# Performance work log

Hardware: AMD Instinct MI355X
Metric: run time of the kernel (lower is better)

The kernel has to match this reference:

```python
import jax, jax.numpy as jnp
import numpy as np

N = 8192
N_DIM = 7
N_WIDTH = 64


def setup_inputs() -> dict:
    key = jax.random.key(0)
    ks = jax.random.split(key, 12)
    scale = 0.05
    u = lambda k, shape: scale * (2.0 * jax.random.uniform(k, shape) - 1.0)
    # Linear params stored as (in, out) so forward uses x @ W + b (same math as torch Linear).
    lin = lambda k, fan_in, fan_out: (
        jax.random.uniform(jax.random.fold_in(k, 0), (fan_in, fan_out),
                           minval=-1.0, maxval=1.0) / np.sqrt(fan_in),
        jax.random.uniform(jax.random.fold_in(k, 1), (fan_out,),
                           minval=-1.0, maxval=1.0) / np.sqrt(fan_in),
    )
    W1, b1 = lin(ks[1], N_DIM, N_WIDTH)
    W2, b2 = lin(ks[2], N_WIDTH, N_WIDTH)
    Wl, bl = lin(ks[3], N_WIDTH, 1)
    return {
        "x": jax.random.normal(ks[0], (N, N_DIM), dtype=jnp.float32),
        "alpha": jax.random.uniform(ks[4], (1,)),          # Edges.alpha = 1 * rand(1)
        "W1": W1, "b1": b1, "wt1": u(ks[5], (N_WIDTH, N_WIDTH)), "bs1": u(ks[6], (1,)),
        "W2": W2, "b2": b2, "wt2": u(ks[7], (N_WIDTH, N_WIDTH)), "bs2": u(ks[8], (1,)),
        "Wl": Wl, "bl": bl,
    }


def _edges(x, alpha):
    eta, phi = x[:, 1], x[:, 2]
    deta = eta[:, None] - eta[None, :]                      # (n, n)
    dphi = jnp.abs(phi[:, None] - phi[None, :])
    dphi = jnp.where(dphi > jnp.pi, 2.0 * jnp.pi - dphi, dphi)
    dRdR = deta * deta + dphi * dphi
    A = jnp.exp(-alpha[0] * dRdR)
    return jax.nn.softmax(A, axis=1) + jnp.eye(x.shape[0], dtype=x.dtype)


def _gcn_layer(X, A, W, b, wt, bs):
    X = jax.nn.relu(X @ W + b)                              # embed + relu
    X = (A @ X) @ wt + bs[0]                                # aggregate + mix + scalar bias
    return jax.nn.relu(X)


def reference(x, alpha, W1, b1, wt1, bs1, W2, b2, wt2, bs2, Wl, bl):
    A = _edges(x, alpha)
    V = jax.nn.relu(_gcn_layer(x, A, W1, b1, wt1, bs1))
    V = jax.nn.relu(_gcn_layer(V, A, W2, b2, wt2, bs2))
    s = V.sum(axis=0)                                       # (n_width,)
    return jax.nn.sigmoid(s @ Wl + bl)                      # (1,)
```

## Files before the change

kernel.cpp:

```cpp
#include <hip/hip_runtime.h>
#include <math.h>

#define NN 8192
#define L2E 1.44269504088896340736f
#define TWO_PI 6.28318530717958647693f

typedef _Float16 h8 __attribute__((ext_vector_type(8)));
typedef _Float16 h4 __attribute__((ext_vector_type(4)));
typedef float f32x4 __attribute__((ext_vector_type(4)));
typedef float f32x2 __attribute__((ext_vector_type(2)));
#define MFMA16(A, B, C) __builtin_amdgcn_mfma_f32_16x16x32_f16(A, B, C, 0, 0, 0)

union V8 { float4 v[2]; float f[8]; };

__global__ __launch_bounds__(256) void prep_kernel(
    const float* __restrict__ x, const float* __restrict__ alpha,
    const float* __restrict__ W1, const float* __restrict__ b1,
    float* __restrict__ eta_s, float* __restrict__ phi_s,
    float* __restrict__ H1, _Float16* __restrict__ HT1,
    float* __restrict__ svec)
{
  __shared__ float sW[448];
  __shared__ float sb[64];
  __shared__ float T[32][68];
  const int t = threadIdx.x;
  if (blockIdx.x == 0 && t < 64) svec[t] = 0.f;
  for (int k = t; k < 448; k += 256) sW[k] = W1[k];
  if (t < 64) sb[t] = b1[t];
  const float s = sqrtf(alpha[0] * L2E);
  const int i0 = blockIdx.x * 32;
  const int r = t >> 3, q = t & 7;
  const int i = i0 + r;
  float xv[7];
#pragma unroll
  for (int k = 0; k < 7; k++) xv[k] = x[i * 7 + k];
  if (q == 0) { eta_s[i] = xv[1] * s; phi_s[i] = xv[2] * s; }
  __syncthreads();
#pragma unroll
  for (int c = 0; c < 8; c++) {
    const int n = q * 8 + c;
    float hv = sb[n];
#pragma unroll
    for (int k = 0; k < 7; k++) hv = fmaf(xv[k], sW[k * 64 + n], hv);
    T[r][n] = fmaxf(hv, 0.f);
  }
  __syncthreads();
  for (int e = t; e < 512; e += 256)
    *(f32x4*)(H1 + (size_t)i0 * 64 + (e << 2)) =
        *(const f32x4*)&T[e >> 4][(e << 2) & 63];
  const int n = t >> 2, sg = (t & 3) * 8;
  h8 v;
#pragma unroll
  for (int ss = 0; ss < 8; ss++) v[ss] = (_Float16)T[sg + ss][n];
  *(h8*)(HT1 + (size_t)n * NN + i0 + sg) = v;
}

template <bool NEED_L>
__global__ __launch_bounds__(256, 4) void attn_pass(
    const float* __restrict__ eta_s, const float* __restrict__ phi_s,
    const _Float16* __restrict__ HT, const float* __restrict__ alpha,
    float* __restrict__ Ypart, float* __restrict__ lpart)
{
  __shared__ __align__(16) float smem[2 * 32 * 66];
  const int tid = threadIdx.x;
  const int w = tid >> 6, lane = tid & 63, m = lane & 15, g = lane >> 4;
  const int tile = blockIdx.x >> 2, part = blockIdx.x & 3;
  const int i0 = tile << 5;
  const int jbase = part << 11;
  const float Cs = TWO_PI * sqrtf(alpha[0] * L2E);
  const float et0 = eta_s[i0 + m],      ph0 = phi_s[i0 + m];
  const float et1 = eta_s[i0 + 16 + m], ph1 = phi_s[i0 + 16 + m];

  const int joff = jbase + (w << 5) + (g << 3);
  const _Float16* hb0 = HT + (size_t)m * NN + joff;
  const _Float16* hb1 = hb0 + (size_t)16 * NN;
  const _Float16* hb2 = hb0 + (size_t)32 * NN;
  const _Float16* hb3 = hb0 + (size_t)48 * NN;
  const float* ep = eta_s + joff;
  const float* pp = phi_s + joff;

  f32x4 a00 = {0,0,0,0}, a01 = {0,0,0,0}, a02 = {0,0,0,0}, a03 = {0,0,0,0};
  f32x4 a10 = {0,0,0,0}, a11 = {0,0,0,0}, a12 = {0,0,0,0}, a13 = {0,0,0,0};
  f32x4 l0a = {0,0,0,0}, l1a = {0,0,0,0};
  const h8 onesv = {(_Float16)1.f, (_Float16)1.f, (_Float16)1.f, (_Float16)1.f,
                    (_Float16)1.f, (_Float16)1.f, (_Float16)1.f, (_Float16)1.f};

  union AF { h8 v; decltype(__builtin_amdgcn_cvt_pkrtz(0.f, 0.f)) p[4]; };

#pragma unroll
  for (int s = 0; s < 16; ++s) {
    const h8 b0 = *(const h8*)(hb0 + s * 128);
    const h8 b1 = *(const h8*)(hb1 + s * 128);
    const h8 b2 = *(const h8*)(hb2 + s * 128);
    const h8 b3 = *(const h8*)(hb3 + s * 128);
    V8 E, P;
    E.v[0] = *(const float4*)(ep + s * 128);
    E.v[1] = *(const float4*)(ep + s * 128 + 4);
    P.v[0] = *(const float4*)(pp + s * 128);
    P.v[1] = *(const float4*)(pp + s * 128 + 4);

    AF af0, af1;
#pragma unroll
    for (int tt = 0; tt < 8; tt += 2) {
      const f32x2 pj = {P.f[tt], P.f[tt + 1]};
      const f32x2 ej = {E.f[tt], E.f[tt + 1]};
      const f32x2 dp0 = ph0 - pj, dp1 = ph1 - pj;
      const f32x2 ad0 = {fabsf(dp0.x), fabsf(dp0.y)};
      const f32x2 ad1 = {fabsf(dp1.x), fabsf(dp1.y)};
      const f32x2 cm0 = Cs - ad0, cm1 = Cs - ad1;
      const f32x2 wr0 = {fminf(ad0.x, cm0.x), fminf(ad0.y, cm0.y)};
      const f32x2 wr1 = {fminf(ad1.x, cm1.x), fminf(ad1.y, cm1.y)};
      const f32x2 de0 = et0 - ej, de1 = et1 - ej;
      const f32x2 r20 = de0 * de0 + wr0 * wr0;
      const f32x2 r21 = de1 * de1 + wr1 * wr1;
      const f32x2 ax0 = {__builtin_amdgcn_exp2f(-r20.x),
                         __builtin_amdgcn_exp2f(-r20.y)};
      const f32x2 ax1 = {__builtin_amdgcn_exp2f(-r21.x),
                         __builtin_amdgcn_exp2f(-r21.y)};
      const f32x2 ga0 = ax0 * L2E - L2E;
      const f32x2 ga1 = ax1 * L2E - L2E;
      af0.p[tt >> 1] = __builtin_amdgcn_cvt_pkrtz(
          __builtin_amdgcn_exp2f(ga0.x), __builtin_amdgcn_exp2f(ga0.y));
      af1.p[tt >> 1] = __builtin_amdgcn_cvt_pkrtz(
          __builtin_amdgcn_exp2f(ga1.x), __builtin_amdgcn_exp2f(ga1.y));
    }
    a00 = MFMA16(af0.v, b0, a00); a01 = MFMA16(af0.v, b1, a01);
    a02 = MFMA16(af0.v, b2, a02); a03 = MFMA16(af0.v, b3, a03);
    a10 = MFMA16(af1.v, b0, a10); a11 = MFMA16(af1.v, b1, a11);
    a12 = MFMA16(af1.v, b2, a12); a13 = MFMA16(af1.v, b3, a13);
    if constexpr (NEED_L) {
      l0a = MFMA16(af0.v, onesv, l0a);
      l1a = MFMA16(af1.v, onesv, l1a);
    }
  }

  typedef float Red2[32][66];
  Red2* red = (Red2*)smem;
  const int h = w >> 1;
  if ((w & 1) == 0) {
#pragma unroll
    for (int r = 0; r < 4; ++r) {
      red[h][g * 4 + r][m]      = a00[r]; red[h][g * 4 + r][16 + m] = a01[r];
      red[h][g * 4 + r][32 + m] = a02[r]; red[h][g * 4 + r][48 + m] = a03[r];
      red[h][16 + g * 4 + r][m]      = a10[r]; red[h][16 + g * 4 + r][16 + m] = a11[r];
      red[h][16 + g * 4 + r][32 + m] = a12[r]; red[h][16 + g * 4 + r][48 + m] = a13[r];
    }
    if constexpr (NEED_L) {
      if (m == 0) {
#pragma unroll
        for (int r = 0; r < 4; ++r) {
          red[h][g * 4 + r][64]      = l0a[r];
          red[h][16 + g * 4 + r][64] = l1a[r];
        }
      }
    }
  }
  __syncthreads();
  if (w & 1) {
#pragma unroll
    for (int r = 0; r < 4; ++r) {
      red[h][g * 4 + r][m]      += a00[r]; red[h][g * 4 + r][16 + m] += a01[r];
      red[h][g * 4 + r][32 + m] += a02[r]; red[h][g * 4 + r][48 + m] += a03[r];
      red[h][16 + g * 4 + r][m]      += a10[r]; red[h][16 + g * 4 + r][16 + m] += a11[r];
      red[h][16 + g * 4 + r][32 + m] += a12[r]; red[h][16 + g * 4 + r][48 + m] += a13[r];
    }
    if constexpr (NEED_L) {
      if (m == 0) {
#pragma unroll
        for (int r = 0; r < 4; ++r) {
          red[h][g * 4 + r][64]      += l0a[r];
          red[h][16 + g * 4 + r][64] += l1a[r];
        }
      }
    }
  }
  __syncthreads();
#pragma unroll
  for (int k = 0; k < 8; ++k) {
    const int e = tid + k * 256;
    Ypart[((size_t)part * NN + i0 + (e >> 6)) * 64 + (e & 63)] =
        red[0][e >> 6][e & 63] + red[1][e >> 6][e & 63];
  }
  if constexpr (NEED_L) {
    if (tid < 32)
      lpart[(size_t)part * NN + i0 + tid] = red[0][tid][64] + red[1][tid][64];
  }
}

__global__ __launch_bounds__(256) void mid_kernel(
    const float* __restrict__ Yp, const float* __restrict__ lp,
    const float* __restrict__ H1, const float* __restrict__ wt1,
    const float* __restrict__ bs1, const float* __restrict__ W2,
    const float* __restrict__ b2, float* __restrict__ H2,
    _Float16* __restrict__ HT2)
{
  __shared__ float sA[64][68];
  __shared__ float sB[64][68];
  __shared__ float U[16][68];
  __shared__ float sb2v[64];
  const int t = threadIdx.x;
  for (int e = t; e < 1024; e += 256) {
    const int rr = e >> 4, cc = (e << 2) & 63;
    *(f32x4*)&sA[rr][cc] = *(const f32x4*)(wt1 + (e << 2));
    *(f32x4*)&sB[rr][cc] = *(const f32x4*)(W2 + (e << 2));
  }
  if (t < 64) sb2v[t] = b2[t];
  const float bsv = bs1[0];
  const int i0 = blockIdx.x * 16;
  const int r = t >> 4, q = t & 15;
  const int i = i0 + r;
  float l = 0.f;
#pragma unroll
  for (int p = 0; p < 4; ++p) l += lp[(size_t)p * NN + i];
  const float rl = 1.0f / l;
  f32x4 ya = {0, 0, 0, 0};
#pragma unroll
  for (int p = 0; p < 4; ++p)
    ya += *(const f32x4*)(Yp + ((size_t)p * NN + i) * 64 + q * 4);
  const f32x4 h1 = *(const f32x4*)(H1 + (size_t)i * 64 + q * 4);
#pragma unroll
  for (int c = 0; c < 4; ++c) U[r][q * 4 + c] = fmaf(ya[c], rl, h1[c]);
  __syncthreads();
  float z[4];
#pragma unroll
  for (int c = 0; c < 4; ++c) z[c] = bsv;
#pragma unroll
  for (int k4 = 0; k4 < 64; k4 += 4) {
    const f32x4 u4 = *(const f32x4*)&U[r][k4];
#pragma unroll
    for (int kk = 0; kk < 4; ++kk) {
      const f32x4 sa = *(const f32x4*)&sA[k4 + kk][q * 4];
#pragma unroll
      for (int c = 0; c < 4; ++c) z[c] = fmaf(u4[kk], sa[c], z[c]);
    }
  }
  __syncthreads();
#pragma unroll
  for (int c = 0; c < 4; ++c) U[r][q * 4 + c] = fmaxf(z[c], 0.f);
  __syncthreads();
  float hv[4];
#pragma unroll
  for (int c = 0; c < 4; ++c) hv[c] = sb2v[q * 4 + c];
#pragma unroll
  for (int k4 = 0; k4 < 64; k4 += 4) {
    const f32x4 u4 = *(const f32x4*)&U[r][k4];
#pragma unroll
    for (int kk = 0; kk < 4; ++kk) {
      const f32x4 sb4 = *(const f32x4*)&sB[k4 + kk][q * 4];
#pragma unroll
      for (int c = 0; c < 4; ++c) hv[c] = fmaf(u4[kk], sb4[c], hv[c]);
    }
  }
  __syncthreads();
#pragma unroll
  for (int c = 0; c < 4; ++c) U[r][q * 4 + c] = fmaxf(hv[c], 0.f);
  __syncthreads();
  *(f32x4*)(H2 + (size_t)i0 * 64 + (t << 2)) =
      *(const f32x4*)&U[t >> 4][(t << 2) & 63];
  const int n = t >> 2, sg = (t & 3) * 4;
  h4 v;
#pragma unroll
  for (int ss = 0; ss < 4; ss++) v[ss] = (_Float16)U[sg + ss][n];
  *(h4*)(HT2 + (size_t)n * NN + i0 + sg) = v;
}

__global__ __launch_bounds__(256) void final_kernel(
    const float* __restrict__ Yp, const float* __restrict__ lp,
    const float* __restrict__ H2, const float* __restrict__ wt2,
    const float* __restrict__ bs2, float* __restrict__ svec)
{
  __shared__ float sA[64][68];
  __shared__ float U[16][68];
  __shared__ float cred[4][64];
  const int t = threadIdx.x;
  for (int e = t; e < 1024; e += 256) {
    const int rr = e >> 4, cc = (e << 2) & 63;
    *(f32x4*)&sA[rr][cc] = *(const f32x4*)(wt2 + (e << 2));
  }
  const float bsv = bs2[0];
  const int i0 = blockIdx.x * 16;
  const int r = t >> 4, q = t & 15;
  const int i = i0 + r;
  float l = 0.f;
#pragma unroll
  for (int p = 0; p < 4; ++p) l += lp[(size_t)p * NN + i];
  const float rl = 1.0f / l;
  f32x4 ya = {0, 0, 0, 0};
#pragma unroll
  for (int p = 0; p < 4; ++p)
    ya += *(const f32x4*)(Yp + ((size_t)p * NN + i) * 64 + q * 4);
  const f32x4 h2 = *(const f32x4*)(H2 + (size_t)i * 64 + q * 4);
#pragma unroll
  for (int c = 0; c < 4; ++c) U[r][q * 4 + c] = fmaf(ya[c], rl, h2[c]);
  __syncthreads();
  float z[4];
#pragma unroll
  for (int c = 0; c < 4; ++c) z[c] = bsv;
#pragma unroll
  for (int k4 = 0; k4 < 64; k4 += 4) {
    const f32x4 u4 = *(const f32x4*)&U[r][k4];
#pragma unroll
    for (int kk = 0; kk < 4; ++kk) {
      const f32x4 sa = *(const f32x4*)&sA[k4 + kk][q * 4];
#pragma unroll
      for (int c = 0; c < 4; ++c) z[c] = fmaf(u4[kk], sa[c], z[c]);
    }
  }
  __syncthreads();
#pragma unroll
  for (int c = 0; c < 4; ++c) U[r][q * 4 + c] = fmaxf(z[c], 0.f);
  __syncthreads();
  const int col = t & 63, rg = t >> 6;
  float ps = 0.f;
#pragma unroll
  for (int rr = 0; rr < 4; rr++) ps += U[rg * 4 + rr][col];
  cred[rg][col] = ps;
  __syncthreads();
  if (t < 64)
    atomicAdd(svec + t, cred[0][t] + cred[1][t] + cred[2][t] + cred[3][t]);
}

__global__ void out_kernel(const float* __restrict__ svec,
                           const float* __restrict__ Wl,
                           const float* __restrict__ bl,
                           float* __restrict__ out)
{
  const int t = threadIdx.x;
  float v = svec[t] * Wl[t];
#pragma unroll
  for (int off = 32; off > 0; off >>= 1) v += __shfl_down(v, off);
  if (t == 0) {
    const float logit = v + bl[0];
    out[0] = 1.0f / (1.0f + __builtin_amdgcn_exp2f(-logit * L2E));
  }
}

extern "C" void kernel_launch(void* const* d_in, const int* in_sizes, int n_in,
                              void* d_out, int out_size, void* d_ws,
                              size_t ws_size, hipStream_t stream)
{
  const float* x     = (const float*)d_in[0];
  const float* alpha = (const float*)d_in[1];
  const float* W1    = (const float*)d_in[2];
  const float* b1    = (const float*)d_in[3];
  const float* wt1   = (const float*)d_in[4];
  const float* bs1   = (const float*)d_in[5];
  const float* W2    = (const float*)d_in[6];
  const float* b2    = (const float*)d_in[7];
  const float* wt2   = (const float*)d_in[8];
  const float* bs2   = (const float*)d_in[9];
  const float* Wl    = (const float*)d_in[10];
  const float* bl    = (const float*)d_in[11];
  float* out = (float*)d_out;

  char* ws = (char*)d_ws;
  size_t off = 0;
  auto alloc = [&](size_t bytes) {
    void* p = ws + off;
    off = (off + bytes + 255) & ~(size_t)255;
    return p;
  };
  float* eta_s = (float*)alloc(NN * 4 + 256);
  float* phi_s = (float*)alloc(NN * 4 + 256);
  float* H1    = (float*)alloc((size_t)NN * 64 * 4);
  float* H2    = (float*)alloc((size_t)NN * 64 * 4);
  float* Ypart = (float*)alloc((size_t)4 * NN * 64 * 4);
  float* lpart = (float*)alloc((size_t)4 * NN * 4);
  _Float16* HT = (_Float16*)alloc((size_t)NN * 64 * 2 + 512);
  float* svec  = (float*)alloc(64 * 4);

  prep_kernel<<<256, 256, 0, stream>>>(x, alpha, W1, b1, eta_s, phi_s, H1, HT, svec);
  attn_pass<true><<<1024, 256, 0, stream>>>(eta_s, phi_s, HT, alpha, Ypart, lpart);
  mid_kernel<<<512, 256, 0, stream>>>(Ypart, lpart, H1, wt1, bs1, W2, b2, H2, HT);
  attn_pass<false><<<1024, 256, 0, stream>>>(eta_s, phi_s, HT, alpha, Ypart, nullptr);
  final_kernel<<<512, 256, 0, stream>>>(Ypart, lpart, H2, wt2, bs2, svec);
  out_kernel<<<1, 64, 0, stream>>>(svec, Wl, bl, out);
}
```

Before: 187.4 us.

## Double-buffer HT tiles via direct global-to-LDS loads in attention pass

The attention pass now streams the fp16 HT operand tiles into a per-wave double-buffered LDS slab with global_load_lds. The next step's eta/phi values are prefetched into registers while the current step computes, with explicit vmcnt waits and sched barriers controlling the overlap. The goal is to hide global load latency behind the exp/MFMA work. In exchange, the kernel uses 32 KB of shared memory per block, which may limit occupancy against the 4-blocks launch bound, and correctness depends on hand-tuned waitcnt values.

```diff
diff --git a/kernel.cpp b/kernel.cpp
--- a/kernel.cpp
+++ b/kernel.cpp
@@ -10,6 +10,11 @@
 typedef float f32x4 __attribute__((ext_vector_type(4)));
 typedef float f32x2 __attribute__((ext_vector_type(2)));
 #define MFMA16(A, B, C) __builtin_amdgcn_mfma_f32_16x16x32_f16(A, B, C, 0, 0, 0)
+
+#define GLD_LDS16(gsrc, ldst)                                          \
+  __builtin_amdgcn_global_load_lds(                                    \
+      (const __attribute__((address_space(1))) unsigned int*)(gsrc),   \
+      (__attribute__((address_space(3))) unsigned int*)(ldst), 16, 0, 0)
 
 union V8 { float4 v[2]; float f[8]; };
 
@@ -61,7 +66,7 @@
     const _Float16* __restrict__ HT, const float* __restrict__ alpha,
     float* __restrict__ Ypart, float* __restrict__ lpart)
 {
-  __shared__ __align__(16) float smem[2 * 32 * 66];
+  __shared__ __align__(16) char smem[32768];
   const int tid = threadIdx.x;
   const int w = tid >> 6, lane = tid & 63, m = lane & 15, g = lane >> 4;
   const int tile = blockIdx.x >> 2, part = blockIdx.x & 3;
@@ -72,12 +77,11 @@
   const float et1 = eta_s[i0 + 16 + m], ph1 = phi_s[i0 + 16 + m];
 
   const int joff = jbase + (w << 5) + (g << 3);
-  const _Float16* hb0 = HT + (size_t)m * NN + joff;
-  const _Float16* hb1 = hb0 + (size_t)16 * NN;
-  const _Float16* hb2 = hb0 + (size_t)32 * NN;
-  const _Float16* hb3 = hb0 + (size_t)48 * NN;
+  const _Float16* hb = HT + (size_t)m * NN + joff;
   const float* ep = eta_s + joff;
   const float* pp = phi_s + joff;
+
+  char* const slab = smem + (w << 13);
 
   f32x4 a00 = {0,0,0,0}, a01 = {0,0,0,0}, a02 = {0,0,0,0}, a03 = {0,0,0,0};
   f32x4 a10 = {0,0,0,0}, a11 = {0,0,0,0}, a12 = {0,0,0,0}, a13 = {0,0,0,0};
@@ -85,19 +89,42 @@
   const h8 onesv = {(_Float16)1.f, (_Float16)1.f, (_Float16)1.f, (_Float16)1.f,
                     (_Float16)1.f, (_Float16)1.f, (_Float16)1.f, (_Float16)1.f};
 
+  V8 Eb[2], Pb[2];
+
+#pragma unroll
+  for (int k = 0; k < 4; ++k)
+    GLD_LDS16(hb + (size_t)k * 16 * NN, slab + (k << 10));
+  Eb[0].v[0] = *(const float4*)(ep);     Eb[0].v[1] = *(const float4*)(ep + 4);
+  Pb[0].v[0] = *(const float4*)(pp);     Pb[0].v[1] = *(const float4*)(pp + 4);
+  __builtin_amdgcn_sched_barrier(0);
+
   union AF { h8 v; decltype(__builtin_amdgcn_cvt_pkrtz(0.f, 0.f)) p[4]; };
 
 #pragma unroll
   for (int s = 0; s < 16; ++s) {
-    const h8 b0 = *(const h8*)(hb0 + s * 128);
-    const h8 b1 = *(const h8*)(hb1 + s * 128);
-    const h8 b2 = *(const h8*)(hb2 + s * 128);
-    const h8 b3 = *(const h8*)(hb3 + s * 128);
-    V8 E, P;
-    E.v[0] = *(const float4*)(ep + s * 128);
-    E.v[1] = *(const float4*)(ep + s * 128 + 4);
-    P.v[0] = *(const float4*)(pp + s * 128);
-    P.v[1] = *(const float4*)(pp + s * 128 + 4);
+    if (s < 15) {
+      char* const nb = slab + (((s + 1) & 1) << 12);
+      const _Float16* src = hb + (s + 1) * 128;
+#pragma unroll
+      for (int k = 0; k < 4; ++k)
+        GLD_LDS16(src + (size_t)k * 16 * NN, nb + (k << 10));
+      Eb[(s + 1) & 1].v[0] = *(const float4*)(ep + (s + 1) * 128);
+      Eb[(s + 1) & 1].v[1] = *(const float4*)(ep + (s + 1) * 128 + 4);
+      Pb[(s + 1) & 1].v[0] = *(const float4*)(pp + (s + 1) * 128);
+      Pb[(s + 1) & 1].v[1] = *(const float4*)(pp + (s + 1) * 128 + 4);
+    }
+    __builtin_amdgcn_sched_barrier(0);
+    if (s < 15) asm volatile("s_waitcnt vmcnt(8)" ::: "memory");
+    else        asm volatile("s_waitcnt vmcnt(0)" ::: "memory");
+    __builtin_amdgcn_sched_barrier(0);
+
+    const char* fb = slab + ((s & 1) << 12) + (lane << 4);
+    const h8 b0 = *(const h8*)(fb);
+    const h8 b1 = *(const h8*)(fb + 1024);
+    const h8 b2 = *(const h8*)(fb + 2048);
+    const h8 b3 = *(const h8*)(fb + 3072);
+    const V8& E = Eb[s & 1];
+    const V8& P = Pb[s & 1];
 
     AF af0, af1;
 #pragma unroll
@@ -134,6 +161,8 @@
     }
   }
 
+  __syncthreads();
+
   typedef float Red2[32][66];
   Red2* red = (Red2*)smem;
   const int h = w >> 1;
```

After: 193.4 us. 3.2% more time.
